# Performance work log

Measured on AMD Instinct MI355X. Metric: run time of the kernel, lower is better.

The kernel has to match this reference:

```python
import jax, jax.numpy as jnp
import numpy as np

DIM = 256
NUM_HEADS = 8
SAMPLE_RATIO = 4
B, H, W = 8, 32, 32
HEAD_DIM = DIM // NUM_HEADS
SCALE = HEAD_DIM ** (-0.5)


def conv1x1(x, w, b):
    # x: [B,C,H,W], w: [O,C], b: [O]  (1x1 conv == per-pixel channel matmul)
    return jnp.einsum('bchw,oc->bohw', x, w) + b[None, :, None, None]


def setup_inputs() -> dict:
    key = jax.random.key(0)
    ks = jax.random.split(key, 16)
    s = 0.02
    x = jax.random.normal(ks[0], (B, DIM, H, W), dtype=jnp.float32)
    # gumbel noise for the two gumbel-softmax gates (sampled once, fed as input)
    u_q = jax.random.uniform(ks[1], (B, SAMPLE_RATIO, H, W), minval=1e-6, maxval=1.0 - 1e-6)
    u_k = jax.random.uniform(ks[2], (B, SAMPLE_RATIO, H, W), minval=1e-6, maxval=1.0 - 1e-6)
    g_q = -jnp.log(-jnp.log(u_q))
    g_k = -jnp.log(-jnp.log(u_k))
    return {
        'x': x,
        'g_q': g_q,
        'g_k': g_k,
        'Wsq': jax.random.normal(ks[3], (SAMPLE_RATIO, DIM)) * s,
        'bsq': jnp.zeros((SAMPLE_RATIO,), jnp.float32),
        'Wsk': jax.random.normal(ks[4], (SAMPLE_RATIO, DIM)) * s,
        'bsk': jnp.zeros((SAMPLE_RATIO,), jnp.float32),
        'Wq': jax.random.normal(ks[5], (DIM, DIM)) * s,
        'bq': jnp.zeros((DIM,), jnp.float32),
        'Wk': jax.random.normal(ks[6], (DIM, DIM)) * s,
        'bk': jnp.zeros((DIM,), jnp.float32),
        'Wv': jax.random.normal(ks[7], (DIM, DIM)) * s,
        'bv': jnp.zeros((DIM,), jnp.float32),
        'Wp': jax.random.normal(ks[8], (DIM, DIM)) * s,
        'bp': jnp.zeros((DIM,), jnp.float32),
    }


def reference(x, g_q, g_k, Wsq, bsq, Wsk, bsk, Wq, bq, Wk, bk, Wv, bv, Wp, bp):
    Bn, C, Hh, Ww = x.shape
    N = Hh * Ww
    # gumbel-softmax (soft, tau=1) gates; keep channel 0 only
    sample_q = jax.nn.softmax(conv1x1(x, Wsq, bsq) + g_q, axis=1)[:, :1]   # [B,1,H,W]
    sample_k = jax.nn.softmax(conv1x1(x, Wsk, bsk) + g_k, axis=1)[:, :1]

    q = (sample_q * conv1x1(x, Wq, bq)).reshape(Bn, NUM_HEADS, HEAD_DIM, N)
    k = (sample_k * conv1x1(x, Wk, bk)).reshape(Bn, NUM_HEADS, HEAD_DIM, N)
    v_full = conv1x1(x, Wv, bv)                                            # shortcut [B,C,H,W]
    v = v_full.reshape(Bn, NUM_HEADS, HEAD_DIM, N)

    # dense attention: scores [B,h,N,N]
    attn = jax.nn.softmax(jnp.einsum('bhdn,bhdm->bhnm', q * SCALE, k), axis=-1)
    out = jnp.einsum('bhnm,bhdm->bhdn', attn, v).reshape(Bn, C, Hh, Ww)

    gated = sample_q * out + (1.0 - sample_q) * v_full
    return conv1x1(gated, Wp, bp)
```

## Files before the change

kernel.cpp:

```cpp
#include <hip/hip_runtime.h>
#include <hip/hip_bf16.h>

typedef __hip_bfloat16 bf16;
typedef __attribute__((ext_vector_type(8))) short short8;
typedef __attribute__((ext_vector_type(4))) short sh4;
typedef __attribute__((ext_vector_type(4))) float f32x4;

static __device__ __forceinline__ float bf2f(bf16 h) { return __bfloat162float(h); }
static __device__ __forceinline__ short f2bfs(float f) {
    bf16 h = __float2bfloat16(f);
    return *reinterpret_cast<short*>(&h);
}
static __device__ __forceinline__ short8 cvt8(float4 a, float4 b) {
    short8 o;
    o[0] = f2bfs(a.x); o[1] = f2bfs(a.y); o[2] = f2bfs(a.z); o[3] = f2bfs(a.w);
    o[4] = f2bfs(b.x); o[5] = f2bfs(b.y); o[6] = f2bfs(b.z); o[7] = f2bfs(b.w);
    return o;
}

constexpr int Bn = 8;
constexpr int C  = 256;
constexpr int N  = 1024;
constexpr int NH = 8;
constexpr int HD = 32;
constexpr int TS = 264;
constexpr float SCALE = 0.17677669529663687f;

__global__ __launch_bounds__(256) void k_prep(
    const float* __restrict__ Wq, const float* __restrict__ Wk,
    const float* __restrict__ Wv, const float* __restrict__ Wp,
    bf16* __restrict__ Wb)
{
    const int tid = threadIdx.x;
    const int mat = blockIdx.x >> 2, seg = blockIdx.x & 3;
    const float* src = (mat == 0) ? Wq : (mat == 1) ? Wk : (mat == 2) ? Wv : Wp;
    short* dst = reinterpret_cast<short*>(Wb) + (size_t)mat * 256 * 256;
#pragma unroll
    for (int i = 0; i < 16; ++i) {
        int f4 = seg * 4096 + i * 256 + tid;
        float4 v = reinterpret_cast<const float4*>(src)[f4];
        sh4 o;
        o[0] = f2bfs(v.x); o[1] = f2bfs(v.y); o[2] = f2bfs(v.z); o[3] = f2bfs(v.w);
        *reinterpret_cast<sh4*>(dst + (size_t)f4 * 4) = o;
    }
}

__global__ __launch_bounds__(256) void k_fused3(
    const float* __restrict__ x, const float* __restrict__ gq, const float* __restrict__ gk,
    const float* __restrict__ Wsq, const float* __restrict__ bsq,
    const float* __restrict__ Wsk, const float* __restrict__ bsk,
    const bf16* __restrict__ Wb,
    const float* __restrict__ bq, const float* __restrict__ bk, const float* __restrict__ bv,
    bf16* __restrict__ qo, bf16* __restrict__ ko, bf16* __restrict__ vo,
    float* __restrict__ sqg)
{
    __shared__ short T[16 * TS];
    __shared__ float sq_lds[16];
    __shared__ float sk_lds[16];

    const int tid  = threadIdx.x;
    const int wave = tid >> 6;
    const int lane = tid & 63;
    const int col  = lane & 15;
    const int quad = lane >> 4;

    const int b  = blockIdx.x >> 6;
    const int n0 = (blockIdx.x & 63) * 16;

    {
        const float* xp = x + (size_t)b * C * N + n0;
        const int cr = tid >> 2;
        const int f  = tid & 3;
#pragma unroll
        for (int p = 0; p < 4; ++p) {
            int c = p * 64 + cr;
            float4 v = *reinterpret_cast<const float4*>(xp + (size_t)c * N + f * 4);
            T[(f * 4 + 0) * TS + c] = f2bfs(v.x);
            T[(f * 4 + 1) * TS + c] = f2bfs(v.y);
            T[(f * 4 + 2) * TS + c] = f2bfs(v.z);
            T[(f * 4 + 3) * TS + c] = f2bfs(v.w);
        }
    }
    __syncthreads();

    if (wave == 0) {
        const float* wsrc = (col < 4) ? (Wsq + col * C) : (Wsk + (col & 3) * C);
        f32x4 ga = {};
#pragma unroll
        for (int k0 = 0; k0 < 256; k0 += 32) {
            float4 w0 = *reinterpret_cast<const float4*>(wsrc + k0 + quad * 8);
            float4 w1 = *reinterpret_cast<const float4*>(wsrc + k0 + quad * 8 + 4);
            short8 af = cvt8(w0, w1);
            short8 b0 = *reinterpret_cast<const short8*>(&T[col * TS + k0 + quad * 8]);
            ga = __builtin_amdgcn_mfma_f32_16x16x32_bf16(af, b0, ga, 0, 0, 0);
        }
        if (quad < 2) {
            const float* bsrc = (quad == 0) ? bsq : bsk;
            const float* gsrc = (quad == 0) ? gq : gk;
            int n = n0 + col;
            float a[4];
#pragma unroll
            for (int r = 0; r < 4; ++r)
                a[r] = ga[r] + bsrc[r] + gsrc[(size_t)b * 4 * N + (size_t)r * N + n];
            float mx = fmaxf(fmaxf(a[0], a[1]), fmaxf(a[2], a[3]));
            float e = 0.f;
#pragma unroll
            for (int r = 0; r < 4; ++r) e += __expf(a[r] - mx);
            float p0 = __expf(a[0] - mx) / e;
            if (quad == 0) { sq_lds[col] = p0; sqg[b * N + n] = p0; }
            else            sk_lds[col] = p0;
        }
    }
    __syncthreads();

    const short* Ws = reinterpret_cast<const short*>(Wb);
    const int mwbase = wave * 192;
    f32x4 acc[12] = {};
#pragma unroll
    for (int k0 = 0; k0 < 256; k0 += 32) {
        short8 b0 = *reinterpret_cast<const short8*>(&T[col * TS + k0 + quad * 8]);
#pragma unroll
        for (int i = 0; i < 12; ++i) {
            int m = mwbase + i * 16;
            const short* wr = Ws + (size_t)(m >> 8) * 65536
                              + (size_t)((m & 255) + col) * 256 + k0 + quad * 8;
            short8 af = *reinterpret_cast<const short8*>(wr);
            acc[i] = __builtin_amdgcn_mfma_f32_16x16x32_bf16(af, b0, acc[i], 0, 0, 0);
        }
    }
    const int n = n0 + col;
#pragma unroll
    for (int i = 0; i < 12; ++i) {
        int m = mwbase + i * 16;
        int mat = m >> 8;
        int cr  = (m & 255) + quad * 4;
        const float* bb = (mat == 0) ? bq : (mat == 1) ? bk : bv;
        float bias[4];
#pragma unroll
        for (int r = 0; r < 4; ++r) bias[r] = bb[cr + r];
        if (mat < 2) {
            float g = (mat == 0) ? sq_lds[col] * SCALE : sk_lds[col];
            short* op = reinterpret_cast<short*>((mat == 0) ? qo : ko) + (size_t)b * N * C;
            sh4 pack;
#pragma unroll
            for (int r = 0; r < 4; ++r) pack[r] = f2bfs((acc[i][r] + bias[r]) * g);
            *reinterpret_cast<sh4*>(op + (size_t)n * C + cr) = pack;
        } else {
            bf16* op = vo + (size_t)b * C * N;
#pragma unroll
            for (int r = 0; r < 4; ++r)
                op[(size_t)(cr + r) * N + n] = __float2bfloat16(acc[i][r] + bias[r]);
        }
    }
}

__global__ __launch_bounds__(256) void k_attn5(
    const bf16* __restrict__ qo, const bf16* __restrict__ ko,
    const bf16* __restrict__ vo, const float* __restrict__ sqg,
    bf16* __restrict__ gt)
{
    __shared__ short P_lds[4][32 * 72];

    const int tid  = threadIdx.x;
    const int wave = tid >> 6;
    const int lane = tid & 63;
    const int col  = lane & 15;
    const int quad = lane >> 4;

    const int b = blockIdx.x >> 6;
    const int h = (blockIdx.x >> 3) & 7;
    const int qbase = (blockIdx.x & 7) * 128 + wave * 32;

    const short* kp = reinterpret_cast<const short*>(ko) + (size_t)b * N * C + h * HD + quad * 8;
    const short* vp = reinterpret_cast<const short*>(vo) + (size_t)b * C * N + (size_t)h * HD * N;

    short8 qf[2];
    {
        const short* qp = reinterpret_cast<const short*>(qo) + (size_t)b * N * C + h * HD + quad * 8;
#pragma unroll
        for (int g = 0; g < 2; ++g)
            qf[g] = *reinterpret_cast<const short8*>(qp + (size_t)(qbase + g * 16 + col) * C);
    }

    float l[2] = {};
    f32x4 oac[2][2] = {};
    short* P = P_lds[wave];

    short8 kf[4];
#pragma unroll
    for (int c = 0; c < 4; ++c)
        kf[c] = *reinterpret_cast<const short8*>(kp + (size_t)(c * 16 + col) * C);

    for (int kb = 0; kb < N; kb += 64) {
        short8 vf[2][2];
#pragma unroll
        for (int kg = 0; kg < 2; ++kg)
#pragma unroll
            for (int dh = 0; dh < 2; ++dh)
                vf[kg][dh] = *reinterpret_cast<const short8*>(vp + (size_t)(dh * 16 + col) * N + kb + kg * 32 + quad * 8);

#pragma unroll
        for (int g = 0; g < 2; ++g) {
            float s[16];
#pragma unroll
            for (int c = 0; c < 4; ++c) {
                f32x4 acc = {};
                acc = __builtin_amdgcn_mfma_f32_16x16x32_bf16(kf[c], qf[g], acc, 0, 0, 0);
#pragma unroll
                for (int r = 0; r < 4; ++r) s[c * 4 + r] = acc[r];
            }
            float p[16], lloc = 0.f;
#pragma unroll
            for (int i = 0; i < 16; ++i) { p[i] = __expf(s[i]); lloc += p[i]; }
            lloc += __shfl_xor(lloc, 16, 64);
            lloc += __shfl_xor(lloc, 32, 64);
            l[g] += lloc;
#pragma unroll
            for (int c = 0; c < 4; ++c) {
                sh4 pk;
#pragma unroll
                for (int r = 0; r < 4; ++r) pk[r] = f2bfs(p[c * 4 + r]);
                *reinterpret_cast<sh4*>(&P[(g * 16 + col) * 72 + c * 16 + quad * 4]) = pk;
            }
        }

        const int kn = (kb + 64) & (N - 1);
#pragma unroll
        for (int c = 0; c < 4; ++c)
            kf[c] = *reinterpret_cast<const short8*>(kp + (size_t)(kn + c * 16 + col) * C);

#pragma unroll
        for (int kg = 0; kg < 2; ++kg) {
#pragma unroll
            for (int g = 0; g < 2; ++g) {
                short8 pf = *reinterpret_cast<const short8*>(&P[(g * 16 + col) * 72 + kg * 32 + quad * 8]);
#pragma unroll
                for (int dh = 0; dh < 2; ++dh)
                    oac[g][dh] = __builtin_amdgcn_mfma_f32_16x16x32_bf16(vf[kg][dh], pf, oac[g][dh], 0, 0, 0);
            }
        }
    }

#pragma unroll
    for (int g = 0; g < 2; ++g) {
        const int q = qbase + g * 16 + col;
        const float invl = 1.f / l[g];
        const float sqv  = sqg[b * N + q];
        const float hv   = 1.f - sqv;
        short* gp = reinterpret_cast<short*>(gt) + ((size_t)b * N + q) * C + h * HD + quad * 4;
#pragma unroll
        for (int dh = 0; dh < 2; ++dh) {
            sh4 pack;
#pragma unroll
            for (int r = 0; r < 4; ++r) {
                int d = dh * 16 + quad * 4 + r;
                float vb = bf2f(*reinterpret_cast<const bf16*>(vp + (size_t)d * N + q));
                pack[r] = f2bfs(sqv * (oac[g][dh][r] * invl) + hv * vb);
            }
            *reinterpret_cast<sh4*>(gp + dh * 16) = pack;
        }
    }
}

__global__ __launch_bounds__(256) void k_projm2(
    const bf16* __restrict__ gt, const bf16* __restrict__ Wpb,
    const float* __restrict__ bp, float* __restrict__ out)
{
    const int tid  = threadIdx.x;
    const int wave = tid >> 6, lane = tid & 63;
    const int col  = lane & 15, quad = lane >> 4;
    const int mrow = blockIdx.x * 64;
    const int b    = blockIdx.z;
    const int n0   = blockIdx.y * 32;

    const short* Wm = reinterpret_cast<const short*>(Wpb);
    const short* gp = reinterpret_cast<const short*>(gt) + (size_t)b * N * C;
    const int m16 = mrow + wave * 16;

    f32x4 acc[2] = {};
#pragma unroll
    for (int k0 = 0; k0 < 256; k0 += 32) {
        short8 af = *reinterpret_cast<const short8*>(Wm + (size_t)(m16 + col) * 256 + k0 + quad * 8);
#pragma unroll
        for (int cf = 0; cf < 2; ++cf) {
            short8 bfr = *reinterpret_cast<const short8*>(gp + (size_t)(n0 + cf * 16 + col) * C + k0 + quad * 8);
            acc[cf] = __builtin_amdgcn_mfma_f32_16x16x32_bf16(af, bfr, acc[cf], 0, 0, 0);
        }
    }

    float bias[4];
#pragma unroll
    for (int r = 0; r < 4; ++r) bias[r] = bp[m16 + quad * 4 + r];
    float* op = out + (size_t)b * C * N;
#pragma unroll
    for (int cf = 0; cf < 2; ++cf) {
        int n = n0 + cf * 16 + col;
#pragma unroll
        for (int r = 0; r < 4; ++r) {
            int c = m16 + quad * 4 + r;
            op[(size_t)c * N + n] = acc[cf][r] + bias[r];
        }
    }
}

extern "C" void kernel_launch(void* const* d_in, const int* in_sizes, int n_in,
                              void* d_out, int out_size, void* d_ws, size_t ws_size,
                              hipStream_t stream)
{
    const float* x   = (const float*)d_in[0];
    const float* gq  = (const float*)d_in[1];
    const float* gk  = (const float*)d_in[2];
    const float* Wsq = (const float*)d_in[3];
    const float* bsq = (const float*)d_in[4];
    const float* Wsk = (const float*)d_in[5];
    const float* bsk = (const float*)d_in[6];
    const float* Wq  = (const float*)d_in[7];
    const float* bq  = (const float*)d_in[8];
    const float* Wk  = (const float*)d_in[9];
    const float* bk  = (const float*)d_in[10];
    const float* Wv  = (const float*)d_in[11];
    const float* bv  = (const float*)d_in[12];
    const float* Wp  = (const float*)d_in[13];
    const float* bp  = (const float*)d_in[14];

    char* ws = (char*)d_ws;
    float* sqg = (float*)ws;
    bf16* Wb   = (bf16*)(ws + 32768);
    bf16* qo   = (bf16*)(ws + 32768 + 524288);
    bf16* ko   = qo + (size_t)Bn * N * C;
    bf16* vo   = ko + (size_t)Bn * N * C;
    bf16* gt   = vo + (size_t)Bn * C * N;
    float* out = (float*)d_out;

    k_prep<<<16, 256, 0, stream>>>(Wq, Wk, Wv, Wp, Wb);
    k_fused3<<<512, 256, 0, stream>>>(x, gq, gk, Wsq, bsq, Wsk, bsk,
                                      Wb, bq, bk, bv, qo, ko, vo, sqg);
    k_attn5<<<512, 256, 0, stream>>>(qo, ko, vo, sqg, gt);
    k_projm2<<<dim3(4, 32, 8), 256, 0, stream>>>(gt, Wb + 3 * 65536, bp, out);
}
```

Before: 166.1 us.

## Split attention over key halves and QKV projection over output halves

The attention kernel now splits the key range into two halves, doubling the grid. Each half writes unnormalized fp32 partial outputs and row sums to a workspace, and a new reduce kernel combines them and applies the gated residual. The QKV projection kernel also splits its output channels across two blocks per tile, and writes an extra pixel-major copy of V for the reduce step. The aim is more parallelism and occupancy, at the cost of extra fp32 partial-result traffic, an extra launch, and repeated x loading and gate computation in the projection.

```diff
diff --git a/kernel.cpp b/kernel.cpp
--- a/kernel.cpp
+++ b/kernel.cpp
@@ -10,6 +10,9 @@
 static __device__ __forceinline__ short f2bfs(float f) {
     bf16 h = __float2bfloat16(f);
     return *reinterpret_cast<short*>(&h);
+}
+static __device__ __forceinline__ float s2f(short s) {
+    return bf2f(*reinterpret_cast<bf16*>(&s));
 }
 static __device__ __forceinline__ short8 cvt8(float4 a, float4 b) {
     short8 o;
@@ -52,7 +55,7 @@
     const bf16* __restrict__ Wb,
     const float* __restrict__ bq, const float* __restrict__ bk, const float* __restrict__ bv,
     bf16* __restrict__ qo, bf16* __restrict__ ko, bf16* __restrict__ vo,
-    float* __restrict__ sqg)
+    bf16* __restrict__ v_pm, float* __restrict__ sqg)
 {
     __shared__ short T[16 * TS];
     __shared__ float sq_lds[16];
@@ -64,8 +67,10 @@
     const int col  = lane & 15;
     const int quad = lane >> 4;
 
-    const int b  = blockIdx.x >> 6;
-    const int n0 = (blockIdx.x & 63) * 16;
+    const int b     = blockIdx.x >> 7;
+    const int rest  = blockIdx.x & 127;
+    const int n0    = (rest >> 1) * 16;
+    const int mhalf = rest & 1;
 
     {
         const float* xp = x + (size_t)b * C * N + n0;
@@ -107,20 +112,24 @@
 #pragma unroll
             for (int r = 0; r < 4; ++r) e += __expf(a[r] - mx);
             float p0 = __expf(a[0] - mx) / e;
-            if (quad == 0) { sq_lds[col] = p0; sqg[b * N + n] = p0; }
-            else            sk_lds[col] = p0;
+            if (quad == 0) {
+                sq_lds[col] = p0;
+                if (mhalf == 0) sqg[b * N + n] = p0;
+            } else {
+                sk_lds[col] = p0;
+            }
         }
     }
     __syncthreads();
 
     const short* Ws = reinterpret_cast<const short*>(Wb);
-    const int mwbase = wave * 192;
-    f32x4 acc[12] = {};
+    const int mwbase = mhalf * 384 + wave * 96;
+    f32x4 acc[6] = {};
 #pragma unroll
     for (int k0 = 0; k0 < 256; k0 += 32) {
         short8 b0 = *reinterpret_cast<const short8*>(&T[col * TS + k0 + quad * 8]);
 #pragma unroll
-        for (int i = 0; i < 12; ++i) {
+        for (int i = 0; i < 6; ++i) {
             int m = mwbase + i * 16;
             const short* wr = Ws + (size_t)(m >> 8) * 65536
                               + (size_t)((m & 255) + col) * 256 + k0 + quad * 8;
@@ -130,7 +139,7 @@
     }
     const int n = n0 + col;
 #pragma unroll
-    for (int i = 0; i < 12; ++i) {
+    for (int i = 0; i < 6; ++i) {
         int m = mwbase + i * 16;
         int mat = m >> 8;
         int cr  = (m & 255) + quad * 4;
@@ -147,17 +156,22 @@
             *reinterpret_cast<sh4*>(op + (size_t)n * C + cr) = pack;
         } else {
             bf16* op = vo + (size_t)b * C * N;
-#pragma unroll
-            for (int r = 0; r < 4; ++r)
-                op[(size_t)(cr + r) * N + n] = __float2bfloat16(acc[i][r] + bias[r]);
+            sh4 pack;
+#pragma unroll
+            for (int r = 0; r < 4; ++r) {
+                float v = acc[i][r] + bias[r];
+                op[(size_t)(cr + r) * N + n] = __float2bfloat16(v);
+                pack[r] = f2bfs(v);
+            }
+            *reinterpret_cast<sh4*>(reinterpret_cast<short*>(v_pm) + ((size_t)b * N + n) * C + cr) = pack;
         }
     }
 }
 
 __global__ __launch_bounds__(256) void k_attn5(
     const bf16* __restrict__ qo, const bf16* __restrict__ ko,
-    const bf16* __restrict__ vo, const float* __restrict__ sqg,
-    bf16* __restrict__ gt)
+    const bf16* __restrict__ vo,
+    float* __restrict__ o_part, float* __restrict__ l_part)
 {
     __shared__ short P_lds[4][32 * 72];
 
@@ -167,9 +181,12 @@
     const int col  = lane & 15;
     const int quad = lane >> 4;
 
-    const int b = blockIdx.x >> 6;
-    const int h = (blockIdx.x >> 3) & 7;
-    const int qbase = (blockIdx.x & 7) * 128 + wave * 32;
+    const int khalf = blockIdx.x & 1;
+    const int qt    = (blockIdx.x >> 1) & 7;
+    const int h     = (blockIdx.x >> 4) & 7;
+    const int b     = blockIdx.x >> 7;
+    const int qbase = qt * 128 + wave * 32;
+    const int ks    = khalf * 512;
 
     const short* kp = reinterpret_cast<const short*>(ko) + (size_t)b * N * C + h * HD + quad * 8;
     const short* vp = reinterpret_cast<const short*>(vo) + (size_t)b * C * N + (size_t)h * HD * N;
@@ -189,9 +206,9 @@
     short8 kf[4];
 #pragma unroll
     for (int c = 0; c < 4; ++c)
-        kf[c] = *reinterpret_cast<const short8*>(kp + (size_t)(c * 16 + col) * C);
-
-    for (int kb = 0; kb < N; kb += 64) {
+        kf[c] = *reinterpret_cast<const short8*>(kp + (size_t)(ks + c * 16 + col) * C);
+
+    for (int kb = ks; kb < ks + 512; kb += 64) {
         short8 vf[2][2];
 #pragma unroll
         for (int kg = 0; kg < 2; ++kg)
@@ -224,7 +241,7 @@
             }
         }
 
-        const int kn = (kb + 64) & (N - 1);
+        const int kn = ks + ((kb - ks + 64) & 511);
 #pragma unroll
         for (int c = 0; c < 4; ++c)
             kf[c] = *reinterpret_cast<const short8*>(kp + (size_t)(kn + c * 16 + col) * C);
@@ -244,21 +261,56 @@
 #pragma unroll
     for (int g = 0; g < 2; ++g) {
         const int q = qbase + g * 16 + col;
-        const float invl = 1.f / l[g];
-        const float sqv  = sqg[b * N + q];
-        const float hv   = 1.f - sqv;
-        short* gp = reinterpret_cast<short*>(gt) + ((size_t)b * N + q) * C + h * HD + quad * 4;
+        float* op = o_part + (((size_t)khalf * Bn + b) * N + q) * C + h * HD + quad * 4;
 #pragma unroll
         for (int dh = 0; dh < 2; ++dh) {
-            sh4 pack;
-#pragma unroll
-            for (int r = 0; r < 4; ++r) {
-                int d = dh * 16 + quad * 4 + r;
-                float vb = bf2f(*reinterpret_cast<const bf16*>(vp + (size_t)d * N + q));
-                pack[r] = f2bfs(sqv * (oac[g][dh][r] * invl) + hv * vb);
-            }
-            *reinterpret_cast<sh4*>(gp + dh * 16) = pack;
-        }
+            float4 pack;
+            pack.x = oac[g][dh][0]; pack.y = oac[g][dh][1];
+            pack.z = oac[g][dh][2]; pack.w = oac[g][dh][3];
+            *reinterpret_cast<float4*>(op + dh * 16) = pack;
+        }
+        if (quad == 0)
+            l_part[(((size_t)khalf * Bn + b) * NH + h) * N + q] = l[g];
+    }
+}
+
+__global__ __launch_bounds__(256) void k_reduce(
+    const float* __restrict__ o_part, const float* __restrict__ l_part,
+    const bf16* __restrict__ v_pm, const float* __restrict__ sqg,
+    bf16* __restrict__ gt)
+{
+    const int tid = threadIdx.x;
+    const int P   = blockIdx.x * 16 + (tid >> 4);
+    const int b   = P >> 10;
+    const int q   = P & 1023;
+    const int c0  = (tid & 15) * 16;
+    const int h   = c0 >> 5;
+
+    const float l12 = l_part[(((size_t)0 * Bn + b) * NH + h) * N + q]
+                    + l_part[(((size_t)1 * Bn + b) * NH + h) * N + q];
+    const float invl = 1.f / l12;
+    const float sqv = sqg[b * N + q];
+    const float hv  = 1.f - sqv;
+
+    const float* o1 = o_part + ((size_t)b * N + q) * C + c0;
+    const float* o2 = o_part + (((size_t)Bn + b) * N + q) * C + c0;
+    const short* vp = reinterpret_cast<const short*>(v_pm) + ((size_t)b * N + q) * C + c0;
+    short* gp = reinterpret_cast<short*>(gt) + ((size_t)b * N + q) * C + c0;
+
+#pragma unroll
+    for (int u = 0; u < 2; ++u) {
+        short8 vv = *reinterpret_cast<const short8*>(vp + u * 8);
+        short8 og;
+#pragma unroll
+        for (int j = 0; j < 8; j += 4) {
+            float4 a = *reinterpret_cast<const float4*>(o1 + u * 8 + j);
+            float4 c = *reinterpret_cast<const float4*>(o2 + u * 8 + j);
+            og[j + 0] = f2bfs(sqv * ((a.x + c.x) * invl) + hv * s2f(vv[j + 0]));
+            og[j + 1] = f2bfs(sqv * ((a.y + c.y) * invl) + hv * s2f(vv[j + 1]));
+            og[j + 2] = f2bfs(sqv * ((a.z + c.z) * invl) + hv * s2f(vv[j + 2]));
+            og[j + 3] = f2bfs(sqv * ((a.w + c.w) * invl) + hv * s2f(vv[j + 3]));
+        }
+        *reinterpret_cast<short8*>(gp + u * 8) = og;
     }
 }
 
@@ -324,17 +376,22 @@
     const float* bp  = (const float*)d_in[14];
 
     char* ws = (char*)d_ws;
-    float* sqg = (float*)ws;
-    bf16* Wb   = (bf16*)(ws + 32768);
-    bf16* qo   = (bf16*)(ws + 32768 + 524288);
-    bf16* ko   = qo + (size_t)Bn * N * C;
-    bf16* vo   = ko + (size_t)Bn * N * C;
-    bf16* gt   = vo + (size_t)Bn * C * N;
+    size_t off = 0;
+    float* sqg = (float*)(ws + off);            off += 32768;
+    bf16* Wb   = (bf16*)(ws + off);             off += 524288;
+    bf16* qo   = (bf16*)(ws + off);             off += (size_t)Bn * N * C * 2;
+    bf16* ko   = (bf16*)(ws + off);             off += (size_t)Bn * N * C * 2;
+    bf16* vo   = (bf16*)(ws + off);             off += (size_t)Bn * C * N * 2;
+    bf16* v_pm = (bf16*)(ws + off);             off += (size_t)Bn * N * C * 2;
+    float* o_part = (float*)(ws + off);         off += (size_t)2 * Bn * N * C * 4;
+    float* l_part = (float*)(ws + off);         off += (size_t)2 * Bn * NH * N * 4;
+    bf16* gt   = (bf16*)(ws + off);             off += (size_t)Bn * N * C * 2;
     float* out = (float*)d_out;
 
     k_prep<<<16, 256, 0, stream>>>(Wq, Wk, Wv, Wp, Wb);
-    k_fused3<<<512, 256, 0, stream>>>(x, gq, gk, Wsq, bsq, Wsk, bsk,
-                                      Wb, bq, bk, bv, qo, ko, vo, sqg);
-    k_attn5<<<512, 256, 0, stream>>>(qo, ko, vo, sqg, gt);
+    k_fused3<<<1024, 256, 0, stream>>>(x, gq, gk, Wsq, bsq, Wsk, bsk,
+                                       Wb, bq, bk, bv, qo, ko, vo, v_pm, sqg);
+    k_attn5<<<1024, 256, 0, stream>>>(qo, ko, vo, o_part, l_part);
+    k_reduce<<<512, 256, 0, stream>>>(o_part, l_part, v_pm, sqg, gt);
     k_projm2<<<dim3(4, 32, 8), 256, 0, stream>>>(gt, Wb + 3 * 65536, bp, out);
 }
```

Result: slower. 173.5 us (+4.5%).

## Retile QKV projection: 32 pixels per block, split output channels across two blocks

Applied to the files above, without the earlier changes.

The fused gate+QKV kernel now handles 32 pixels per block instead of 16, with each block computing half of the 768 output channels (two blocks per pixel tile). Each weight fragment loaded from global memory now feeds two MFMAs, one per 16-pixel column group, which doubles weight reuse and halves weight traffic per pixel. In exchange, the x tile load and the gumbel gate computation are duplicated across the two channel halves, and only one half writes the gate output.

```diff
diff --git a/kernel.cpp b/kernel.cpp
--- a/kernel.cpp
+++ b/kernel.cpp
@@ -45,7 +45,7 @@
     }
 }
 
-__global__ __launch_bounds__(256) void k_fused3(
+__global__ __launch_bounds__(256) void k_fused4(
     const float* __restrict__ x, const float* __restrict__ gq, const float* __restrict__ gk,
     const float* __restrict__ Wsq, const float* __restrict__ bsq,
     const float* __restrict__ Wsk, const float* __restrict__ bsk,
@@ -54,9 +54,9 @@
     bf16* __restrict__ qo, bf16* __restrict__ ko, bf16* __restrict__ vo,
     float* __restrict__ sqg)
 {
-    __shared__ short T[16 * TS];
-    __shared__ float sq_lds[16];
-    __shared__ float sk_lds[16];
+    __shared__ short T[32 * TS];
+    __shared__ float sq_lds[32];
+    __shared__ float sk_lds[32];
 
     const int tid  = threadIdx.x;
     const int wave = tid >> 6;
@@ -64,16 +64,18 @@
     const int col  = lane & 15;
     const int quad = lane >> 4;
 
-    const int b  = blockIdx.x >> 6;
-    const int n0 = (blockIdx.x & 63) * 16;
+    const int b     = blockIdx.x >> 6;
+    const int rest  = blockIdx.x & 63;
+    const int n0    = (rest >> 1) * 32;
+    const int mhalf = rest & 1;
 
     {
         const float* xp = x + (size_t)b * C * N + n0;
-        const int cr = tid >> 2;
-        const int f  = tid & 3;
-#pragma unroll
-        for (int p = 0; p < 4; ++p) {
-            int c = p * 64 + cr;
+        const int row = tid >> 3;
+        const int f   = tid & 7;
+#pragma unroll
+        for (int p = 0; p < 8; ++p) {
+            int c = p * 32 + row;
             float4 v = *reinterpret_cast<const float4*>(xp + (size_t)c * N + f * 4);
             T[(f * 4 + 0) * TS + c] = f2bfs(v.x);
             T[(f * 4 + 1) * TS + c] = f2bfs(v.y);
@@ -85,53 +87,63 @@
 
     if (wave == 0) {
         const float* wsrc = (col < 4) ? (Wsq + col * C) : (Wsk + (col & 3) * C);
-        f32x4 ga = {};
+        f32x4 ga[2] = {};
 #pragma unroll
         for (int k0 = 0; k0 < 256; k0 += 32) {
             float4 w0 = *reinterpret_cast<const float4*>(wsrc + k0 + quad * 8);
             float4 w1 = *reinterpret_cast<const float4*>(wsrc + k0 + quad * 8 + 4);
             short8 af = cvt8(w0, w1);
             short8 b0 = *reinterpret_cast<const short8*>(&T[col * TS + k0 + quad * 8]);
-            ga = __builtin_amdgcn_mfma_f32_16x16x32_bf16(af, b0, ga, 0, 0, 0);
+            short8 b1 = *reinterpret_cast<const short8*>(&T[(16 + col) * TS + k0 + quad * 8]);
+            ga[0] = __builtin_amdgcn_mfma_f32_16x16x32_bf16(af, b0, ga[0], 0, 0, 0);
+            ga[1] = __builtin_amdgcn_mfma_f32_16x16x32_bf16(af, b1, ga[1], 0, 0, 0);
         }
         if (quad < 2) {
             const float* bsrc = (quad == 0) ? bsq : bsk;
             const float* gsrc = (quad == 0) ? gq : gk;
-            int n = n0 + col;
-            float a[4];
-#pragma unroll
-            for (int r = 0; r < 4; ++r)
-                a[r] = ga[r] + bsrc[r] + gsrc[(size_t)b * 4 * N + (size_t)r * N + n];
-            float mx = fmaxf(fmaxf(a[0], a[1]), fmaxf(a[2], a[3]));
-            float e = 0.f;
-#pragma unroll
-            for (int r = 0; r < 4; ++r) e += __expf(a[r] - mx);
-            float p0 = __expf(a[0] - mx) / e;
-            if (quad == 0) { sq_lds[col] = p0; sqg[b * N + n] = p0; }
-            else            sk_lds[col] = p0;
+#pragma unroll
+            for (int cf = 0; cf < 2; ++cf) {
+                int n = n0 + cf * 16 + col;
+                float a[4];
+#pragma unroll
+                for (int r = 0; r < 4; ++r)
+                    a[r] = ga[cf][r] + bsrc[r] + gsrc[(size_t)b * 4 * N + (size_t)r * N + n];
+                float mx = fmaxf(fmaxf(a[0], a[1]), fmaxf(a[2], a[3]));
+                float e = 0.f;
+#pragma unroll
+                for (int r = 0; r < 4; ++r) e += __expf(a[r] - mx);
+                float p0 = __expf(a[0] - mx) / e;
+                if (quad == 0) {
+                    sq_lds[cf * 16 + col] = p0;
+                    if (mhalf == 0) sqg[b * N + n] = p0;
+                } else {
+                    sk_lds[cf * 16 + col] = p0;
+                }
+            }
         }
     }
     __syncthreads();
 
     const short* Ws = reinterpret_cast<const short*>(Wb);
-    const int mwbase = wave * 192;
-    f32x4 acc[12] = {};
+    const int mbase = mhalf * 384 + wave * 96;
+    f32x4 acc[6][2] = {};
 #pragma unroll
     for (int k0 = 0; k0 < 256; k0 += 32) {
         short8 b0 = *reinterpret_cast<const short8*>(&T[col * TS + k0 + quad * 8]);
-#pragma unroll
-        for (int i = 0; i < 12; ++i) {
-            int m = mwbase + i * 16;
+        short8 b1 = *reinterpret_cast<const short8*>(&T[(16 + col) * TS + k0 + quad * 8]);
+#pragma unroll
+        for (int i = 0; i < 6; ++i) {
+            int m = mbase + i * 16;
             const short* wr = Ws + (size_t)(m >> 8) * 65536
                               + (size_t)((m & 255) + col) * 256 + k0 + quad * 8;
             short8 af = *reinterpret_cast<const short8*>(wr);
-            acc[i] = __builtin_amdgcn_mfma_f32_16x16x32_bf16(af, b0, acc[i], 0, 0, 0);
-        }
-    }
-    const int n = n0 + col;
-#pragma unroll
-    for (int i = 0; i < 12; ++i) {
-        int m = mwbase + i * 16;
+            acc[i][0] = __builtin_amdgcn_mfma_f32_16x16x32_bf16(af, b0, acc[i][0], 0, 0, 0);
+            acc[i][1] = __builtin_amdgcn_mfma_f32_16x16x32_bf16(af, b1, acc[i][1], 0, 0, 0);
+        }
+    }
+#pragma unroll
+    for (int i = 0; i < 6; ++i) {
+        int m = mbase + i * 16;
         int mat = m >> 8;
         int cr  = (m & 255) + quad * 4;
         const float* bb = (mat == 0) ? bq : (mat == 1) ? bk : bv;
@@ -139,17 +151,26 @@
 #pragma unroll
         for (int r = 0; r < 4; ++r) bias[r] = bb[cr + r];
         if (mat < 2) {
-            float g = (mat == 0) ? sq_lds[col] * SCALE : sk_lds[col];
             short* op = reinterpret_cast<short*>((mat == 0) ? qo : ko) + (size_t)b * N * C;
-            sh4 pack;
-#pragma unroll
-            for (int r = 0; r < 4; ++r) pack[r] = f2bfs((acc[i][r] + bias[r]) * g);
-            *reinterpret_cast<sh4*>(op + (size_t)n * C + cr) = pack;
+#pragma unroll
+            for (int cf = 0; cf < 2; ++cf) {
+                int n = n0 + cf * 16 + col;
+                float g = (mat == 0) ? sq_lds[cf * 16 + col] * SCALE
+                                     : sk_lds[cf * 16 + col];
+                sh4 pack;
+#pragma unroll
+                for (int r = 0; r < 4; ++r) pack[r] = f2bfs((acc[i][cf][r] + bias[r]) * g);
+                *reinterpret_cast<sh4*>(op + (size_t)n * C + cr) = pack;
+            }
         } else {
             bf16* op = vo + (size_t)b * C * N;
 #pragma unroll
-            for (int r = 0; r < 4; ++r)
-                op[(size_t)(cr + r) * N + n] = __float2bfloat16(acc[i][r] + bias[r]);
+            for (int cf = 0; cf < 2; ++cf) {
+                int n = n0 + cf * 16 + col;
+#pragma unroll
+                for (int r = 0; r < 4; ++r)
+                    op[(size_t)(cr + r) * N + n] = __float2bfloat16(acc[i][cf][r] + bias[r]);
+            }
         }
     }
 }
@@ -333,7 +354,7 @@
     float* out = (float*)d_out;
 
     k_prep<<<16, 256, 0, stream>>>(Wq, Wk, Wv, Wp, Wb);
-    k_fused3<<<512, 256, 0, stream>>>(x, gq, gk, Wsq, bsq, Wsk, bsk,
+    k_fused4<<<512, 256, 0, stream>>>(x, gq, gk, Wsq, bsq, Wsk, bsk,
                                       Wb, bq, bk, bv, qo, ko, vo, sqg);
     k_attn5<<<512, 256, 0, stream>>>(qo, ko, vo, sqg, gt);
     k_projm2<<<dim3(4, 32, 8), 256, 0, stream>>>(gt, Wb + 3 * 65536, bp, out);
```

New measurement: 153.3 us. -7.7%, faster.
